# Kernel optimization log

Hardware: AMD Instinct MI355X
Metric: run time of the kernel (lower is better)

## Reference

```python
import jax, jax.numpy as jnp
import numpy as np

ALPHA, BETA, GAMMA = 0.1, 0.15, 0.005
W1, W2, SHIFT = 10.0, 3.0, 0.0


def _pairwise_sq_dist(x):
    # x: [B, C, N] -> [B, N, N] of sum_c (x[..,n] - x[..,m])^2, computed cdist-style
    # to avoid materializing the [B, C, N, N] broadcasted intermediate.
    sq = jnp.sum(x * x, axis=1)                      # [B, N]
    gram = jnp.einsum('bcn,bcm->bnm', x, x)          # [B, N, N]
    d = sq[:, :, None] + sq[:, None, :] - 2.0 * gram
    return jnp.maximum(d, 0.0)


def setup_inputs() -> dict:
    key = jax.random.key(0)
    k1, k2, k3 = jax.random.split(key, 3)
    B, CG, CF, H, W, N = 8, 3, 128, 224, 224, 2048
    guidance = jax.random.normal(k1, (B, CG, H, W), dtype=jnp.float32)
    features = jax.random.normal(k2, (B, CF, H, W), dtype=jnp.float32)
    coords = jax.random.randint(k3, (2, N), 0, H)    # H == W == 224
    return {"guidance": guidance, "features": features, "coords": coords}


def reference(guidance, features, coords):
    H, W = guidance.shape[2], guidance.shape[3]
    # normalized coordinates: [2, N]
    norm_coords = coords.astype(jnp.float32) / jnp.array([[H], [W]], dtype=jnp.float32)
    # coord_diff: [1, N, N]
    coord_diff = jnp.sum(
        (norm_coords[:, :, None] - norm_coords[:, None, :]) ** 2, axis=0
    )[None]

    # gather sampled pixels: [B, C, N]
    sel_guidance = guidance[:, :, coords[0], coords[1]]
    sel_feats = features[:, :, coords[0], coords[1]]

    guidance_diff = _pairwise_sq_dist(sel_guidance)  # [B, N, N]
    feat_diff = _pairwise_sq_dist(sel_feats)         # [B, N, N]

    sim_kernel = (
        W1 * jnp.exp(-coord_diff / (2.0 * ALPHA) - guidance_diff / (2.0 * BETA))
        + W2 * jnp.exp(-coord_diff / (2.0 * GAMMA))
        - SHIFT
    )
    return jnp.mean(feat_diff * sim_kernel)
```

## Files before the change

kernel.cpp:

```cpp
#include <hip/hip_runtime.h>
#include <hip/hip_bf16.h>

#define BATCH 8
#define CGUID 3
#define CFEAT 128
#define IMH 224
#define IMW 224
#define NPTS 2048
#define HWSZ (IMH * IMW)

#define TILES 16
#define NPAIR 136
#define BM 128
#define BK 64
#define LDT 72

typedef __attribute__((ext_vector_type(8))) short bf16x8;
typedef __attribute__((ext_vector_type(4))) float f32x4;

__device__ __forceinline__ ushort f2bf(float f) {
  unsigned x = __float_as_uint(f);
  unsigned r = (x + 0x7fffu + ((x >> 16) & 1u)) >> 16;
  return (ushort)r;
}
__device__ __forceinline__ float bf2f(ushort u) {
  return __uint_as_float(((unsigned)u) << 16);
}

__global__ __launch_bounds__(256) void sort_kernel(
    const int* __restrict__ coords,
    int* __restrict__ slin, float2* __restrict__ sc2,
    float* __restrict__ sq, float* __restrict__ out)
{
  __shared__ int ys[NPTS], xs[NPTS];
  __shared__ int hist[IMH], offs[IMH];
  int t = threadIdx.x;
  for (int i = t; i < IMH; i += 256) hist[i] = 0;
  __syncthreads();
  for (int i = t; i < NPTS; i += 256) {
    int y = coords[i], x = coords[NPTS + i];
    ys[i] = y; xs[i] = x;
    atomicAdd(&hist[y], 1);
  }
  __syncthreads();
  if (t == 0) {
    int run = 0;
    for (int i = 0; i < IMH; ++i) { offs[i] = run; run += hist[i]; }
  }
  __syncthreads();
  for (int i = t; i < NPTS; i += 256) {
    int y = ys[i], x = xs[i];
    int r = atomicAdd(&offs[y], 1);
    slin[r] = y * IMW + x;
    sc2[r] = make_float2((float)y / 224.0f, (float)x / 224.0f);
  }
  for (int i = t; i < BATCH * NPTS; i += 256) sq[i] = 0.0f;
  if (t == 0) out[0] = 0.0f;
}

__global__ __launch_bounds__(256) void gather_kernel(
    const float* __restrict__ features, const float* __restrict__ guidance,
    const int* __restrict__ slin,
    ushort* __restrict__ selT, float4* __restrict__ gxyz, float* __restrict__ sq)
{
  int blk = blockIdx.x;
  int cg = blk & 7, pg = (blk >> 3) & 7, b = blk >> 6;
  int t = threadIdx.x;
  int p = pg * 256 + t;
  int lin = slin[p];
  const float* fb = features + (size_t)b * CFEAT * HWSZ + lin;
  float s = 0.0f;
  #pragma unroll
  for (int i = 0; i < 16; ++i) {
    int c = cg * 16 + i;
    float v = fb[(size_t)c * HWSZ];
    ushort u = f2bf(v);
    float fv = bf2f(u);
    s += fv * fv;
    selT[((size_t)(b * CFEAT + c)) * NPTS + p] = u;
  }
  atomicAdd(&sq[b * NPTS + p], s);
  if (cg == 0) {
    const float* gb = guidance + (size_t)b * CGUID * HWSZ + lin;
    gxyz[b * NPTS + p] = make_float4(gb[0], gb[HWSZ], gb[2 * HWSZ], 0.0f);
  }
}

__global__ __launch_bounds__(256) void transpose_kernel(
    const ushort* __restrict__ selT, ushort* __restrict__ selF)
{
  __shared__ ushort Ls[CFEAT][LDT];
  int blk = blockIdx.x;
  int b = blk >> 5, nt = blk & 31;
  int nb = nt * 64;
  int t = threadIdx.x;
  #pragma unroll
  for (int pass = 0; pass < 4; ++pass) {
    int idx = pass * 256 + t;
    int c = idx >> 3, q = idx & 7;
    int4 v = *(const int4*)(selT + ((size_t)(b * CFEAT + c)) * NPTS + nb + q * 8);
    *(int4*)(&Ls[c][q * 8]) = v;
  }
  __syncthreads();
  #pragma unroll
  for (int pass = 0; pass < 4; ++pass) {
    int idx = pass * 256 + t;
    int n = idx >> 4, q = idx & 15;
    unsigned w0 = (unsigned)Ls[q * 8 + 0][n] | ((unsigned)Ls[q * 8 + 1][n] << 16);
    unsigned w1 = (unsigned)Ls[q * 8 + 2][n] | ((unsigned)Ls[q * 8 + 3][n] << 16);
    unsigned w2 = (unsigned)Ls[q * 8 + 4][n] | ((unsigned)Ls[q * 8 + 5][n] << 16);
    unsigned w3 = (unsigned)Ls[q * 8 + 6][n] | ((unsigned)Ls[q * 8 + 7][n] << 16);
    int4 o; o.x = (int)w0; o.y = (int)w1; o.z = (int)w2; o.w = (int)w3;
    *(int4*)(selF + ((size_t)(b * NPTS + nb + n)) * CFEAT + q * 8) = o;
  }
}

__global__ __launch_bounds__(256) void crf_kernel(
    const ushort* __restrict__ selF, const float4* __restrict__ gxyz,
    const float* __restrict__ sq, const float2* __restrict__ sc2,
    float* __restrict__ out)
{
  __shared__ ushort As[BM * LDT];
  __shared__ ushort Bs[BM * LDT];
  __shared__ float4 egN[BM], egM[BM];
  __shared__ float2 ecN[BM], ecM[BM];
  __shared__ float sqN[BM], sqM[BM];
  __shared__ float red[4];

  int b = blockIdx.x / NPAIR;
  int p = blockIdx.x % NPAIR;
  int ti = 0, rem = p;
  while (rem >= TILES - ti) { rem -= TILES - ti; ++ti; }
  int tj = ti + rem;
  int nb0 = ti * BM, mb0 = tj * BM;

  int t = threadIdx.x;
  int lane = t & 63, wid = t >> 6;
  int wr = wid >> 1, wc = wid & 1;

  if (t < BM) {
    egN[t] = gxyz[b * NPTS + nb0 + t];
    sqN[t] = sq[b * NPTS + nb0 + t];
    ecN[t] = sc2[nb0 + t];
  } else {
    int q = t - BM;
    egM[q] = gxyz[b * NPTS + mb0 + q];
    sqM[q] = sq[b * NPTS + mb0 + q];
    ecM[q] = sc2[mb0 + q];
  }

  f32x4 acc[4][4];
  #pragma unroll
  for (int i = 0; i < 4; ++i)
    #pragma unroll
    for (int j = 0; j < 4; ++j) acc[i][j] = (f32x4)0.f;

  const ushort* SA = selF + ((size_t)b * NPTS + nb0) * CFEAT;
  const ushort* SB = selF + ((size_t)b * NPTS + mb0) * CFEAT;

  for (int kk = 0; kk < 2; ++kk) {
    __syncthreads();
    #pragma unroll
    for (int pass = 0; pass < 4; ++pass) {
      int idx = t + pass * 256;
      int row = idx >> 3, q = idx & 7;
      int4 va = *(const int4*)(SA + (size_t)row * CFEAT + kk * BK + q * 8);
      *(int4*)(&As[row * LDT + q * 8]) = va;
      int4 vb = *(const int4*)(SB + (size_t)row * CFEAT + kk * BK + q * 8);
      *(int4*)(&Bs[row * LDT + q * 8]) = vb;
    }
    __syncthreads();
    #pragma unroll
    for (int k2 = 0; k2 < 2; ++k2) {
      int kb = k2 * 32 + (lane >> 4) * 8;
      bf16x8 a[4], bv[4];
      #pragma unroll
      for (int i = 0; i < 4; ++i)
        a[i] = *(const bf16x8*)(&As[(wr * 64 + i * 16 + (lane & 15)) * LDT + kb]);
      #pragma unroll
      for (int j = 0; j < 4; ++j)
        bv[j] = *(const bf16x8*)(&Bs[(wc * 64 + j * 16 + (lane & 15)) * LDT + kb]);
      #pragma unroll
      for (int i = 0; i < 4; ++i)
        #pragma unroll
        for (int j = 0; j < 4; ++j)
          acc[i][j] = __builtin_amdgcn_mfma_f32_16x16x32_bf16(a[i], bv[j], acc[i][j], 0, 0, 0);
    }
  }

  float sum = 0.f;
  int mlo = lane & 15, nhi = lane >> 4;
  #pragma unroll
  for (int i = 0; i < 4; ++i) {
    #pragma unroll
    for (int r = 0; r < 4; ++r) {
      int n = wr * 64 + i * 16 + nhi * 4 + r;
      float4 gn = egN[n];
      float2 cn = ecN[n];
      float sn = sqN[n];
      #pragma unroll
      for (int j = 0; j < 4; ++j) {
        int m = wc * 64 + j * 16 + mlo;
        float4 gm = egM[m];
        float2 cm = ecM[m];
        float df = sn + sqM[m] - 2.0f * acc[i][j][r];
        df = fmaxf(df, 0.0f);
        float d0 = gn.x - gm.x, d1 = gn.y - gm.y, d2 = gn.z - gm.z;
        float dg = d0 * d0 + d1 * d1 + d2 * d2;
        float dy = cn.x - cm.x, dx = cn.y - cm.y;
        float dc = dy * dy + dx * dx;
        float sim = 10.0f * __expf(-5.0f * dc - 3.3333333f * dg)
                  +  3.0f * __expf(-100.0f * dc);
        sum += df * sim;
      }
    }
  }

  #pragma unroll
  for (int o = 32; o > 0; o >>= 1) sum += __shfl_down(sum, o);
  if (lane == 0) red[wid] = sum;
  __syncthreads();
  if (t == 0) {
    float tot = red[0] + red[1] + red[2] + red[3];
    float factor = (ti == tj ? 1.0f : 2.0f) * (1.0f / (8.0f * 2048.0f * 2048.0f));
    atomicAdd(out, tot * factor);
  }
}

extern "C" void kernel_launch(void* const* d_in, const int* in_sizes, int n_in,
                              void* d_out, int out_size, void* d_ws, size_t ws_size,
                              hipStream_t stream) {
  const float* guidance = (const float*)d_in[0];
  const float* features = (const float*)d_in[1];
  const int*   coords   = (const int*)d_in[2];
  float* out = (float*)d_out;

  char* ws = (char*)d_ws;
  size_t off = 0;
  ushort* selT = (ushort*)(ws + off); off += (size_t)BATCH * CFEAT * NPTS * 2;
  ushort* selF = (ushort*)(ws + off); off += (size_t)BATCH * NPTS * CFEAT * 2;
  float4* gxyz = (float4*)(ws + off); off += (size_t)BATCH * NPTS * 16;
  float*  sqv  = (float*) (ws + off); off += (size_t)BATCH * NPTS * 4;
  float2* sc2  = (float2*)(ws + off); off += (size_t)NPTS * 8;
  int*    slin = (int*)   (ws + off); off += (size_t)NPTS * 4;

  sort_kernel<<<1, 256, 0, stream>>>(coords, slin, sc2, sqv, out);
  gather_kernel<<<BATCH * 8 * 8, 256, 0, stream>>>(features, guidance, slin,
                                                   selT, gxyz, sqv);
  transpose_kernel<<<BATCH * 32, 256, 0, stream>>>(selT, selF);
  crf_kernel<<<BATCH * NPAIR, 256, 0, stream>>>(selF, gxyz, sqv, sc2, out);
}
```

Before: 313.1 us.

## Fuse gather and transpose into one kernel, pack squared norms into guidance float4

The gather kernel now writes point-major bf16 feature rows directly, using 16-byte stores of eight channels. This removes the separate transpose kernel and the selT intermediate buffer. Per-point squared norms are reduced in shared memory instead of with global atomics and stored in the w component of the guidance float4, so the zeroing pass and the separate sq loads in the CRF kernel go away. In exchange, the gather launches fewer blocks (256 instead of 512), and each thread issues 32 strided global reads, which may cut the parallelism available for the random-access gather.

```diff
diff --git a/kernel.cpp b/kernel.cpp
--- a/kernel.cpp
+++ b/kernel.cpp
@@ -29,8 +29,7 @@
 
 __global__ __launch_bounds__(256) void sort_kernel(
     const int* __restrict__ coords,
-    int* __restrict__ slin, float2* __restrict__ sc2,
-    float* __restrict__ sq, float* __restrict__ out)
+    int* __restrict__ slin, float2* __restrict__ sc2, float* __restrict__ out)
 {
   __shared__ int ys[NPTS], xs[NPTS];
   __shared__ int hist[IMH], offs[IMH];
@@ -54,77 +53,61 @@
     slin[r] = y * IMW + x;
     sc2[r] = make_float2((float)y / 224.0f, (float)x / 224.0f);
   }
-  for (int i = t; i < BATCH * NPTS; i += 256) sq[i] = 0.0f;
   if (t == 0) out[0] = 0.0f;
 }
 
-__global__ __launch_bounds__(256) void gather_kernel(
+__global__ __launch_bounds__(256) void gatherT_kernel(
     const float* __restrict__ features, const float* __restrict__ guidance,
     const int* __restrict__ slin,
-    ushort* __restrict__ selT, float4* __restrict__ gxyz, float* __restrict__ sq)
+    ushort* __restrict__ selF, float4* __restrict__ g4)
 {
+  __shared__ float sq4[4][64];
   int blk = blockIdx.x;
-  int cg = blk & 7, pg = (blk >> 3) & 7, b = blk >> 6;
+  int b = blk >> 5, pg = blk & 31;
   int t = threadIdx.x;
-  int p = pg * 256 + t;
+  int tq = t >> 6, lane = t & 63;
+  int p = pg * 64 + lane;
   int lin = slin[p];
-  const float* fb = features + (size_t)b * CFEAT * HWSZ + lin;
+
+  const float* fb = features + (size_t)b * CFEAT * HWSZ
+                             + (size_t)(tq * 32) * HWSZ + lin;
+  ushort* rowp = selF + ((size_t)(b * NPTS + p)) * CFEAT + tq * 32;
+
   float s = 0.0f;
   #pragma unroll
-  for (int i = 0; i < 16; ++i) {
-    int c = cg * 16 + i;
-    float v = fb[(size_t)c * HWSZ];
-    ushort u = f2bf(v);
-    float fv = bf2f(u);
-    s += fv * fv;
-    selT[((size_t)(b * CFEAT + c)) * NPTS + p] = u;
-  }
-  atomicAdd(&sq[b * NPTS + p], s);
-  if (cg == 0) {
+  for (int cc = 0; cc < 32; cc += 8) {
+    ushort u[8];
+    #pragma unroll
+    for (int k = 0; k < 8; ++k) {
+      float v = fb[(size_t)(cc + k) * HWSZ];
+      u[k] = f2bf(v);
+      float fv = bf2f(u[k]);
+      s += fv * fv;
+    }
+    int4 o;
+    o.x = (int)((unsigned)u[0] | ((unsigned)u[1] << 16));
+    o.y = (int)((unsigned)u[2] | ((unsigned)u[3] << 16));
+    o.z = (int)((unsigned)u[4] | ((unsigned)u[5] << 16));
+    o.w = (int)((unsigned)u[6] | ((unsigned)u[7] << 16));
+    *(int4*)(rowp + cc) = o;
+  }
+  sq4[tq][lane] = s;
+  __syncthreads();
+  if (tq == 0) {
+    float tot = sq4[0][lane] + sq4[1][lane] + sq4[2][lane] + sq4[3][lane];
     const float* gb = guidance + (size_t)b * CGUID * HWSZ + lin;
-    gxyz[b * NPTS + p] = make_float4(gb[0], gb[HWSZ], gb[2 * HWSZ], 0.0f);
-  }
-}
-
-__global__ __launch_bounds__(256) void transpose_kernel(
-    const ushort* __restrict__ selT, ushort* __restrict__ selF)
-{
-  __shared__ ushort Ls[CFEAT][LDT];
-  int blk = blockIdx.x;
-  int b = blk >> 5, nt = blk & 31;
-  int nb = nt * 64;
-  int t = threadIdx.x;
-  #pragma unroll
-  for (int pass = 0; pass < 4; ++pass) {
-    int idx = pass * 256 + t;
-    int c = idx >> 3, q = idx & 7;
-    int4 v = *(const int4*)(selT + ((size_t)(b * CFEAT + c)) * NPTS + nb + q * 8);
-    *(int4*)(&Ls[c][q * 8]) = v;
-  }
-  __syncthreads();
-  #pragma unroll
-  for (int pass = 0; pass < 4; ++pass) {
-    int idx = pass * 256 + t;
-    int n = idx >> 4, q = idx & 15;
-    unsigned w0 = (unsigned)Ls[q * 8 + 0][n] | ((unsigned)Ls[q * 8 + 1][n] << 16);
-    unsigned w1 = (unsigned)Ls[q * 8 + 2][n] | ((unsigned)Ls[q * 8 + 3][n] << 16);
-    unsigned w2 = (unsigned)Ls[q * 8 + 4][n] | ((unsigned)Ls[q * 8 + 5][n] << 16);
-    unsigned w3 = (unsigned)Ls[q * 8 + 6][n] | ((unsigned)Ls[q * 8 + 7][n] << 16);
-    int4 o; o.x = (int)w0; o.y = (int)w1; o.z = (int)w2; o.w = (int)w3;
-    *(int4*)(selF + ((size_t)(b * NPTS + nb + n)) * CFEAT + q * 8) = o;
+    g4[b * NPTS + p] = make_float4(gb[0], gb[HWSZ], gb[2 * HWSZ], tot);
   }
 }
 
 __global__ __launch_bounds__(256) void crf_kernel(
-    const ushort* __restrict__ selF, const float4* __restrict__ gxyz,
-    const float* __restrict__ sq, const float2* __restrict__ sc2,
-    float* __restrict__ out)
+    const ushort* __restrict__ selF, const float4* __restrict__ g4,
+    const float2* __restrict__ sc2, float* __restrict__ out)
 {
   __shared__ ushort As[BM * LDT];
   __shared__ ushort Bs[BM * LDT];
   __shared__ float4 egN[BM], egM[BM];
   __shared__ float2 ecN[BM], ecM[BM];
-  __shared__ float sqN[BM], sqM[BM];
   __shared__ float red[4];
 
   int b = blockIdx.x / NPAIR;
@@ -139,13 +122,11 @@
   int wr = wid >> 1, wc = wid & 1;
 
   if (t < BM) {
-    egN[t] = gxyz[b * NPTS + nb0 + t];
-    sqN[t] = sq[b * NPTS + nb0 + t];
+    egN[t] = g4[b * NPTS + nb0 + t];
     ecN[t] = sc2[nb0 + t];
   } else {
     int q = t - BM;
-    egM[q] = gxyz[b * NPTS + mb0 + q];
-    sqM[q] = sq[b * NPTS + mb0 + q];
+    egM[q] = g4[b * NPTS + mb0 + q];
     ecM[q] = sc2[mb0 + q];
   }
 
@@ -197,13 +178,12 @@
       int n = wr * 64 + i * 16 + nhi * 4 + r;
       float4 gn = egN[n];
       float2 cn = ecN[n];
-      float sn = sqN[n];
       #pragma unroll
       for (int j = 0; j < 4; ++j) {
         int m = wc * 64 + j * 16 + mlo;
         float4 gm = egM[m];
         float2 cm = ecM[m];
-        float df = sn + sqM[m] - 2.0f * acc[i][j][r];
+        float df = gn.w + gm.w - 2.0f * acc[i][j][r];
         df = fmaxf(df, 0.0f);
         float d0 = gn.x - gm.x, d1 = gn.y - gm.y, d2 = gn.z - gm.z;
         float dg = d0 * d0 + d1 * d1 + d2 * d2;
@@ -237,16 +217,13 @@
 
   char* ws = (char*)d_ws;
   size_t off = 0;
-  ushort* selT = (ushort*)(ws + off); off += (size_t)BATCH * CFEAT * NPTS * 2;
   ushort* selF = (ushort*)(ws + off); off += (size_t)BATCH * NPTS * CFEAT * 2;
-  float4* gxyz = (float4*)(ws + off); off += (size_t)BATCH * NPTS * 16;
-  float*  sqv  = (float*) (ws + off); off += (size_t)BATCH * NPTS * 4;
+  float4* g4   = (float4*)(ws + off); off += (size_t)BATCH * NPTS * 16;
   float2* sc2  = (float2*)(ws + off); off += (size_t)NPTS * 8;
   int*    slin = (int*)   (ws + off); off += (size_t)NPTS * 4;
 
-  sort_kernel<<<1, 256, 0, stream>>>(coords, slin, sc2, sqv, out);
-  gather_kernel<<<BATCH * 8 * 8, 256, 0, stream>>>(features, guidance, slin,
-                                                   selT, gxyz, sqv);
-  transpose_kernel<<<BATCH * 32, 256, 0, stream>>>(selT, selF);
-  crf_kernel<<<BATCH * NPAIR, 256, 0, stream>>>(selF, gxyz, sqv, sc2, out);
-}
+  sort_kernel<<<1, 256, 0, stream>>>(coords, slin, sc2, out);
+  gatherT_kernel<<<BATCH * 32, 256, 0, stream>>>(features, guidance, slin,
+                                                 selF, g4);
+  crf_kernel<<<BATCH * NPAIR, 256, 0, stream>>>(selF, g4, sc2, out);
+}
```

After: 311.6 us. About the same (-0.5%).
